# Optimization experiments

Measured on AMD Instinct MI355X. Metric: run time of the kernel, lower is better.

Reference implementation:

```python
import jax, jax.numpy as jnp
import numpy as np
import math

HIDDEN = 1024
HEADS = 16
HEAD_DIM = HIDDEN // HEADS


def setup_inputs() -> dict:
    key = jax.random.key(0)
    ks = jax.random.split(key, 9)
    s = 1.0 / math.sqrt(HIDDEN)
    x = jax.random.normal(ks[0], (4, 2048, HIDDEN), dtype=jnp.float32)
    Wq = jax.random.uniform(ks[1], (HIDDEN, HIDDEN), jnp.float32, -s, s)
    bq = jax.random.uniform(ks[2], (HIDDEN,), jnp.float32, -s, s)
    Wk = jax.random.uniform(ks[3], (HIDDEN, HIDDEN), jnp.float32, -s, s)
    bk = jax.random.uniform(ks[4], (HIDDEN,), jnp.float32, -s, s)
    Wv = jax.random.uniform(ks[5], (HIDDEN, HIDDEN), jnp.float32, -s, s)
    bv = jax.random.uniform(ks[6], (HIDDEN,), jnp.float32, -s, s)
    Wo = jax.random.uniform(ks[7], (HIDDEN, HIDDEN), jnp.float32, -s, s)
    bo = jax.random.uniform(ks[8], (HIDDEN,), jnp.float32, -s, s)
    return {"x": x, "Wq": Wq, "bq": bq, "Wk": Wk, "bk": bk,
            "Wv": Wv, "bv": bv, "Wo": Wo, "bo": bo}


def reference(x, Wq, bq, Wk, bk, Wv, bv, Wo, bo):
    B, T, D = x.shape
    H, Hd = HEADS, HEAD_DIM
    scale = 1.0 / math.sqrt(Hd)
    # projections (torch Linear: y = x @ W.T + b)
    q = (x @ Wq.T + bq).reshape(B, T, H, Hd).transpose(0, 2, 1, 3)  # [B,H,T,Hd]
    k = (x @ Wk.T + bk).reshape(B, T, H, Hd).transpose(0, 2, 1, 3)
    v = (x @ Wv.T + bv).reshape(B, T, H, Hd).transpose(0, 2, 1, 3)
    scores = jnp.einsum("bhqd,bhkd->bhqk", q, k) * scale  # [B,H,T,T]
    attn = jax.nn.softmax(scores, axis=-1)
    out = jnp.einsum("bhqk,bhkd->bhqd", attn, v)  # [B,H,T,Hd]
    out = out.transpose(0, 2, 1, 3).reshape(B, T, D)
    out = out @ Wo.T + bo
    return out.mean(axis=1)  # [B, D]
```

## Files before the change

### kernel.cpp

```cpp
#include <hip/hip_runtime.h>
#include <stdint.h>

#define HIDDEN 1024
#define HEADS 16
#define HEAD_DIM 64
#define BATCH 4
#define SEQ 2048
#define NTOK (BATCH * SEQ)

typedef __attribute__((ext_vector_type(8))) short bf16x8;
typedef __attribute__((ext_vector_type(4))) float floatx4;
typedef __attribute__((ext_vector_type(16))) float floatx16;

#define SCALE_Q 0.18033688011112042f

__device__ __forceinline__ unsigned short f2bf(float f) {
    union { float f; unsigned u; } x; x.f = f;
    unsigned r = x.u + 0x7fffu + ((x.u >> 16) & 1u);
    return (unsigned short)(r >> 16);
}

__device__ __forceinline__ float fast_exp2(float x) {
#if __has_builtin(__builtin_amdgcn_exp2f)
    return __builtin_amdgcn_exp2f(x);
#else
    return exp2f(x);
#endif
}

typedef __attribute__((address_space(3))) unsigned int lds_u32;
typedef const __attribute__((address_space(1))) unsigned int gl_u32;

__device__ __forceinline__ void async_cp16(const void* g, void* l) {
#if __has_builtin(__builtin_amdgcn_global_load_lds)
    __builtin_amdgcn_global_load_lds((gl_u32*)g, (lds_u32*)l, 16, 0, 0);
#else
    *(uint4*)((char*)l + (threadIdx.x & 63) * 16) = *(const uint4*)g;
#endif
}

__global__ __launch_bounds__(256) void conv_all(
    const float* __restrict__ x, const float* __restrict__ Wq,
    const float* __restrict__ Wk, const float* __restrict__ Wv,
    unsigned short* __restrict__ x_bf, unsigned short* __restrict__ wq_bf,
    unsigned short* __restrict__ wk_bf, unsigned short* __restrict__ wv_bf,
    float* __restrict__ accp) {
    const int blk = blockIdx.x, tid = threadIdx.x;
    const float* src;
    unsigned short* dst;
    size_t i;
    if (blk < 8192) {
        src = x; dst = x_bf; i = (size_t)blk * 256 + tid;
        if (blk < 16) accp[blk * 256 + tid] = 0.0f;
    } else {
        int r = blk - 8192;
        int s = r >> 10;
        src = (s == 0) ? Wq : (s == 1) ? Wk : Wv;
        dst = (s == 0) ? wq_bf : (s == 1) ? wk_bf : wv_bf;
        i = (size_t)(r & 1023) * 256 + tid;
    }
    float4 v = *(const float4*)(src + 4 * i);
    unsigned short o[4];
    o[0] = f2bf(v.x); o[1] = f2bf(v.y); o[2] = f2bf(v.z); o[3] = f2bf(v.w);
    *(ushort4*)(dst + 4 * i) = *(ushort4*)o;
}

__global__ __launch_bounds__(256, 3) void qkv_gemm(
    const unsigned short* __restrict__ X,
    const unsigned short* __restrict__ W0, const unsigned short* __restrict__ W1,
    const unsigned short* __restrict__ W2,
    const float* __restrict__ b0, const float* __restrict__ b1,
    const float* __restrict__ b2,
    unsigned short* __restrict__ O0, unsigned short* __restrict__ O1,
    unsigned short* __restrict__ O2) {
    __shared__ __align__(16) char smem[34816];
    unsigned short* tbuf = (unsigned short*)smem;

    const int id = blockIdx.x;
    const int mb = id & 63, nzb = id >> 6;
    const int z = nzb >> 3, nz = nzb & 7;
    const int m0 = mb * 128;
    const unsigned short* W = (z == 0) ? W0 : (z == 1) ? W1 : W2;
    const float* bias       = (z == 0) ? b0 : (z == 1) ? b1 : b2;

    const int tid = threadIdx.x, lane = tid & 63, wave = tid >> 6;
    const int wm = (wave & 1) * 64, wn = (wave >> 1) * 64;

    const int srow = lane >> 2;
    const int sxc = ((lane & 3) ^ (srow & 3)) * 8;
    const unsigned short* ga[2];
    const unsigned short* gb[2];
#pragma unroll
    for (int j = 0; j < 2; ++j) {
        ga[j] = X + (size_t)(m0 + wave * 32 + j * 16 + srow) * HIDDEN + sxc;
        gb[j] = W + (size_t)(nz * 128 + wave * 32 + j * 16 + srow) * HIDDEN + sxc;
    }

    floatx4 acc[4][4];
#pragma unroll
    for (int tm = 0; tm < 4; ++tm)
#pragma unroll
        for (int tn = 0; tn < 4; ++tn)
#pragma unroll
            for (int r = 0; r < 4; ++r) acc[tm][tn][r] = 0.f;

#pragma unroll
    for (int j = 0; j < 2; ++j) {
        async_cp16(ga[j], smem + wave * 2048 + j * 1024);
        async_cp16(gb[j], smem + 16384 + wave * 2048 + j * 1024);
        ga[j] += 32; gb[j] += 32;
    }
    __syncthreads();

    const int fr = (lane & 15) * 64 + (((lane >> 4) ^ (lane & 3)) * 16);
    for (int kt = 0; kt < 32; ++kt) {
        const int cur = kt & 1;
        if (kt < 31) {
#pragma unroll
            for (int j = 0; j < 2; ++j) {
                async_cp16(ga[j], smem + (cur ^ 1) * 8192 + wave * 2048 + j * 1024);
                async_cp16(gb[j], smem + 16384 + (cur ^ 1) * 8192 + wave * 2048 + j * 1024);
                ga[j] += 32; gb[j] += 32;
            }
        }
        const char* Ab = smem + cur * 8192;
        const char* Bb = smem + 16384 + cur * 8192;
        bf16x8 af[4], bfr[4];
#pragma unroll
        for (int t = 0; t < 4; ++t) {
            af[t]  = *(bf16x8*)(Ab + (wm + t * 16) * 64 + fr);
            bfr[t] = *(bf16x8*)(Bb + (wn + t * 16) * 64 + fr);
        }
#pragma unroll
        for (int tm = 0; tm < 4; ++tm)
#pragma unroll
            for (int tn = 0; tn < 4; ++tn)
                acc[tm][tn] = __builtin_amdgcn_mfma_f32_16x16x32_bf16(af[tm], bfr[tn], acc[tm][tn], 0, 0, 0);
        if (kt < 31) __syncthreads();
    }

    const int col = lane & 15, rbase = (lane >> 4) * 4;
    __syncthreads();
    if (z == 2) {
#pragma unroll
        for (int tm = 0; tm < 4; ++tm)
#pragma unroll
            for (int tn = 0; tn < 4; ++tn) {
                const int dr = wn + tn * 16 + col;
                const float bs = bias[nz * 128 + dr];
                const int mi0 = wm + tm * 16 + rbase;
                unsigned short vals[4];
#pragma unroll
                for (int r = 0; r < 4; ++r) vals[r] = f2bf(acc[tm][tn][r] + bs);
                *(ushort4*)&tbuf[dr * 136 + mi0] = *(ushort4*)vals;
            }
        __syncthreads();
        const int dr = tid >> 1, seg = tid & 1;
        const int hh = nz * 2 + (dr >> 6), dd = dr & 63;
        const int bb = m0 >> 11, tb = (m0 & (SEQ - 1)) >> 7;
        unsigned short* dst = O2 + (((size_t)bb * HEADS + hh) * HEAD_DIM + dd) * SEQ
                                 + tb * 128 + seg * 64;
        const unsigned short* srcl = &tbuf[dr * 136 + seg * 64];
#pragma unroll
        for (int i = 0; i < 8; ++i)
            *(uint4*)(dst + i * 8) = *(const uint4*)(srcl + i * 8);
    } else {
        unsigned short* O = (z == 0) ? O0 : O1;
        const float sc = (z == 0) ? SCALE_Q : 1.0f;
#pragma unroll
        for (int tm = 0; tm < 4; ++tm)
#pragma unroll
            for (int tn = 0; tn < 4; ++tn) {
                const int nn = wn + tn * 16 + col;
                const float bs = bias[nz * 128 + nn];
                const int mi0 = wm + tm * 16 + rbase;
#pragma unroll
                for (int r = 0; r < 4; ++r)
                    tbuf[(mi0 + r) * 136 + nn] = f2bf((acc[tm][tn][r] + bs) * sc);
            }
        __syncthreads();
        const int r = tid >> 1, seg = tid & 1;
        unsigned short* dst = O + (size_t)(m0 + r) * HIDDEN + nz * 128 + seg * 64;
        const unsigned short* srcl = &tbuf[r * 136 + seg * 64];
#pragma unroll
        for (int i = 0; i < 8; ++i)
            *(uint4*)(dst + i * 8) = *(const uint4*)(srcl + i * 8);
    }
}

__global__ __launch_bounds__(256, 2) void attn_mfma(
    const unsigned short* __restrict__ Q, const unsigned short* __restrict__ K,
    const unsigned short* __restrict__ Vt, float* __restrict__ accp) {
    __shared__ unsigned short Klds[2][8192];
    __shared__ unsigned short Vlds[2][8192];

    const int tid = threadIdx.x, lane = tid & 63, wave = tid >> 6;
    const int lq = lane & 31, g2 = lane >> 5;

    const int f = blockIdx.x;
    const int bh = (f & 7) * 8 + ((f >> 3) & 7);
    const int qc = f >> 6;
    const int b = bh >> 4, h = bh & 15;

    bf16x8 qfrag[2][4];
#pragma unroll
    for (int g = 0; g < 2; ++g) {
        const size_t qb = ((size_t)(b * SEQ + qc * 256 + wave * 64 + g * 32 + lq)) * HIDDEN
                          + h * HEAD_DIM + g2 * 8;
#pragma unroll
        for (int ds = 0; ds < 4; ++ds) qfrag[g][ds] = *(const bf16x8*)&Q[qb + ds * 16];
    }

    const unsigned short* kg[4];
    const unsigned short* vg[4];
    {
        const int kr = lane >> 3;
        const int kc = ((lane & 7) ^ kr) * 8;
#pragma unroll
        for (int j = 0; j < 4; ++j)
            kg[j] = K + ((size_t)(b * SEQ + wave * 32 + j * 8 + kr)) * HIDDEN + h * HEAD_DIM + kc;
#pragma unroll
        for (int j = 0; j < 4; ++j) {
            const int dl = wave * 16 + j * 4 + (lane >> 4);
            const int cc = ((lane & 15) ^ (dl & 15)) * 8;
            vg[j] = Vt + ((size_t)bh * HEAD_DIM + dl) * SEQ + cc;
        }
    }

    floatx16 oacc[2][2], lacc[2];
#pragma unroll
    for (int g = 0; g < 2; ++g)
#pragma unroll
        for (int r = 0; r < 16; ++r) { oacc[g][0][r] = 0.f; oacc[g][1][r] = 0.f; lacc[g][r] = 0.f; }

    bf16x8 ones;
    {
        union { bf16x8 v; unsigned u[4]; } o;
        o.u[0] = o.u[1] = o.u[2] = o.u[3] = 0x3F803F80u;
        ones = o.v;
    }

#pragma unroll
    for (int j = 0; j < 4; ++j) {
        async_cp16(kg[j], (char*)Klds[0] + (wave * 32 + j * 8) * 128);
        async_cp16(vg[j], (char*)Vlds[0] + (wave * 16 + j * 4) * 256);
        kg[j] += 128 * HIDDEN; vg[j] += 128;
    }
    __syncthreads();

    for (int it = 0; it < 16; ++it) {
        const int cur = it & 1;
        if (it < 15) {
#pragma unroll
            for (int j = 0; j < 4; ++j) {
                async_cp16(kg[j], (char*)Klds[cur ^ 1] + (wave * 32 + j * 8) * 128);
                async_cp16(vg[j], (char*)Vlds[cur ^ 1] + (wave * 16 + j * 4) * 256);
                kg[j] += 128 * HIDDEN; vg[j] += 128;
            }
        }
#pragma unroll
        for (int ks4 = 0; ks4 < 4; ++ks4) {
            const int kk = ks4 * 32;
            const int rr = kk + lq;
            bf16x8 kf[4];
#pragma unroll
            for (int ds = 0; ds < 4; ++ds)
                kf[ds] = *(bf16x8*)((char*)Klds[cur] + rr * 128 + (((g2 + 2 * ds) ^ (lq & 7)) * 16));

            unsigned pk[2][8];
#pragma unroll
            for (int g = 0; g < 2; ++g) {
                floatx16 sacc;
#pragma unroll
                for (int r = 0; r < 16; ++r) sacc[r] = 0.f;
#pragma unroll
                for (int ds = 0; ds < 4; ++ds)
                    sacc = __builtin_amdgcn_mfma_f32_32x32x16_bf16(kf[ds], qfrag[g][ds], sacc, 0, 0, 0);
#pragma unroll
                for (int j = 0; j < 8; ++j) {
                    union { float f; unsigned u; } plo, phi;
                    plo.f = fast_exp2(sacc[2 * j]);
                    phi.f = fast_exp2(sacc[2 * j + 1]);
                    pk[g][j] = __builtin_amdgcn_perm(phi.u, plo.u, 0x07060302u);
                }
            }
#pragma unroll
            for (int ks2 = 0; ks2 < 2; ++ks2) {
                bf16x8 vf[2];
#pragma unroll
                for (int nf = 0; nf < 2; ++nf) {
                    const int d = nf * 32 + lq;
                    const int c0 = (4 * ks4 + 2 * ks2) ^ (d & 15);
                    const int c1 = (4 * ks4 + 2 * ks2 + 1) ^ (d & 15);
                    union { uint2 h[2]; bf16x8 v; } u;
                    u.h[0] = *(uint2*)((char*)Vlds[cur] + d * 256 + c0 * 16 + g2 * 8);
                    u.h[1] = *(uint2*)((char*)Vlds[cur] + d * 256 + c1 * 16 + g2 * 8);
                    vf[nf] = u.v;
                }
#pragma unroll
                for (int g = 0; g < 2; ++g) {
                    union { uint4 u; bf16x8 v; } af;
                    af.u.x = pk[g][4 * ks2];
                    af.u.y = pk[g][4 * ks2 + 1];
                    af.u.z = pk[g][4 * ks2 + 2];
                    af.u.w = pk[g][4 * ks2 + 3];
#pragma unroll
                    for (int nf = 0; nf < 2; ++nf)
                        oacc[g][nf] = __builtin_amdgcn_mfma_f32_32x32x16_bf16(af.v, vf[nf], oacc[g][nf], 0, 0, 0);
                    lacc[g] = __builtin_amdgcn_mfma_f32_32x32x16_bf16(af.v, ones, lacc[g], 0, 0, 0);
                }
            }
        }
        if (it < 15) __syncthreads();
    }

#pragma unroll
    for (int g = 0; g < 2; ++g)
#pragma unroll
        for (int nf = 0; nf < 2; ++nf) {
            float v = 0.f;
#pragma unroll
            for (int r = 0; r < 16; ++r) v += oacc[g][nf][r] / lacc[g][r];
            v += __shfl_xor(v, 32, 64);
            if (lane < 32)
                atomicAdd(&accp[b * HIDDEN + h * HEAD_DIM + nf * 32 + lq], v);
        }
}

__global__ __launch_bounds__(256) void out_proj(const float* __restrict__ acc,
                                                const float* __restrict__ Wo,
                                                const float* __restrict__ bo,
                                                float* __restrict__ out) {
    __shared__ float red[256];
    const int n = blockIdx.x * 64 + (threadIdx.x & 63);
    const int ks = threadIdx.x >> 6;
    const int b = blockIdx.y;
    const float* wr = Wo + (size_t)n * HIDDEN + ks * 256;
    const float* ar = acc + b * HIDDEN + ks * 256;
    float s = 0.f;
#pragma unroll 8
    for (int k = 0; k < 256; k += 4) {
        float4 w = *(const float4*)(wr + k);
        float4 a = *(const float4*)(ar + k);
        s += w.x * a.x + w.y * a.y + w.z * a.z + w.w * a.w;
    }
    red[threadIdx.x] = s;
    __syncthreads();
    if (threadIdx.x < 64) {
        float t = red[threadIdx.x] + red[threadIdx.x + 64]
                + red[threadIdx.x + 128] + red[threadIdx.x + 192];
        out[b * HIDDEN + n] = t * (1.0f / (float)SEQ) + bo[n];
    }
}

extern "C" void kernel_launch(void* const* d_in, const int* in_sizes, int n_in,
                              void* d_out, int out_size, void* d_ws, size_t ws_size,
                              hipStream_t stream) {
    const float* x  = (const float*)d_in[0];
    const float* Wq = (const float*)d_in[1];
    const float* bq = (const float*)d_in[2];
    const float* Wk = (const float*)d_in[3];
    const float* bk = (const float*)d_in[4];
    const float* Wv = (const float*)d_in[5];
    const float* bv = (const float*)d_in[6];
    const float* Wo = (const float*)d_in[7];
    const float* bo = (const float*)d_in[8];
    float* out = (float*)d_out;

    char* ws = (char*)d_ws;
    unsigned short* x_bf  = (unsigned short*)(ws);
    unsigned short* wq_bf = (unsigned short*)(ws + 16777216);
    unsigned short* wk_bf = (unsigned short*)(ws + 18874368);
    unsigned short* wv_bf = (unsigned short*)(ws + 20971520);
    unsigned short* q_bf  = (unsigned short*)(ws + 23068672);
    unsigned short* k_bf  = (unsigned short*)(ws + 39845888);
    unsigned short* vt_bf = (unsigned short*)(ws + 56623104);
    float*          accp  = (float*)(ws + 73400320);

    conv_all<<<dim3(8192 + 3072), dim3(256), 0, stream>>>(
        x, Wq, Wk, Wv, x_bf, wq_bf, wk_bf, wv_bf, accp);

    qkv_gemm<<<dim3(1536), dim3(256), 0, stream>>>(
        x_bf, wq_bf, wk_bf, wv_bf, bq, bk, bv, q_bf, k_bf, vt_bf);

    attn_mfma<<<dim3(512), dim3(256), 0, stream>>>(q_bf, k_bf, vt_bf, accp);

    out_proj<<<dim3(16, BATCH), dim3(256), 0, stream>>>(accp, Wo, bo, out);
}
```

Baseline: 255.4 us.

## Halve attention tile sizes to double blocks and occupancy; permute V-transpose LDS rows

The attention kernel now gives each wave 32 queries instead of 64 and streams 64-key tiles instead of 128. This halves LDS and register use, so launch bounds can target 4 blocks per CU and the grid doubles to 1024 blocks. The V tile layout and swizzle are reworked so each V fragment is one 16-byte LDS read. The QKV GEMM's V-transpose store also permutes row indices to reduce LDS bank conflicts. In exchange, K/V traffic per query doubles, and the loop runs twice as many iterations, each with its own barrier.

```diff
diff --git a/kernel.cpp b/kernel.cpp
--- a/kernel.cpp
+++ b/kernel.cpp
@@ -149,10 +149,11 @@
                 const int dr = wn + tn * 16 + col;
                 const float bs = bias[nz * 128 + dr];
                 const int mi0 = wm + tm * 16 + rbase;
+                const int mip = (mi0 & ~12) | ((mi0 & 4) << 1) | ((mi0 & 8) >> 1);
                 unsigned short vals[4];
 #pragma unroll
                 for (int r = 0; r < 4; ++r) vals[r] = f2bf(acc[tm][tn][r] + bs);
-                *(ushort4*)&tbuf[dr * 136 + mi0] = *(ushort4*)vals;
+                *(ushort4*)&tbuf[dr * 136 + mip] = *(ushort4*)vals;
             }
         __syncthreads();
         const int dr = tid >> 1, seg = tid & 1;
@@ -188,11 +189,11 @@
     }
 }
 
-__global__ __launch_bounds__(256, 2) void attn_mfma(
+__global__ __launch_bounds__(256, 4) void attn_mfma(
     const unsigned short* __restrict__ Q, const unsigned short* __restrict__ K,
     const unsigned short* __restrict__ Vt, float* __restrict__ accp) {
-    __shared__ unsigned short Klds[2][8192];
-    __shared__ unsigned short Vlds[2][8192];
+    __shared__ unsigned short Klds[2][4096];
+    __shared__ unsigned short Vlds[2][4096];
 
     const int tid = threadIdx.x, lane = tid & 63, wave = tid >> 6;
     const int lq = lane & 31, g2 = lane >> 5;
@@ -202,36 +203,33 @@
     const int qc = f >> 6;
     const int b = bh >> 4, h = bh & 15;
 
-    bf16x8 qfrag[2][4];
-#pragma unroll
-    for (int g = 0; g < 2; ++g) {
-        const size_t qb = ((size_t)(b * SEQ + qc * 256 + wave * 64 + g * 32 + lq)) * HIDDEN
+    bf16x8 qfrag[4];
+    {
+        const size_t qb = ((size_t)(b * SEQ + qc * 128 + wave * 32 + lq)) * HIDDEN
                           + h * HEAD_DIM + g2 * 8;
 #pragma unroll
-        for (int ds = 0; ds < 4; ++ds) qfrag[g][ds] = *(const bf16x8*)&Q[qb + ds * 16];
-    }
-
-    const unsigned short* kg[4];
-    const unsigned short* vg[4];
+        for (int ds = 0; ds < 4; ++ds) qfrag[ds] = *(const bf16x8*)&Q[qb + ds * 16];
+    }
+
+    const unsigned short* kg[2];
+    const unsigned short* vg[2];
     {
         const int kr = lane >> 3;
         const int kc = ((lane & 7) ^ kr) * 8;
 #pragma unroll
-        for (int j = 0; j < 4; ++j)
-            kg[j] = K + ((size_t)(b * SEQ + wave * 32 + j * 8 + kr)) * HIDDEN + h * HEAD_DIM + kc;
-#pragma unroll
-        for (int j = 0; j < 4; ++j) {
-            const int dl = wave * 16 + j * 4 + (lane >> 4);
-            const int cc = ((lane & 15) ^ (dl & 15)) * 8;
+        for (int j = 0; j < 2; ++j)
+            kg[j] = K + ((size_t)(b * SEQ + wave * 16 + j * 8 + kr)) * HIDDEN + h * HEAD_DIM + kc;
+#pragma unroll
+        for (int j = 0; j < 2; ++j) {
+            const int dl = wave * 16 + j * 8 + (lane >> 3);
+            const int cc = ((lane & 7) ^ (dl & 7)) * 8;
             vg[j] = Vt + ((size_t)bh * HEAD_DIM + dl) * SEQ + cc;
         }
     }
 
-    floatx16 oacc[2][2], lacc[2];
-#pragma unroll
-    for (int g = 0; g < 2; ++g)
-#pragma unroll
-        for (int r = 0; r < 16; ++r) { oacc[g][0][r] = 0.f; oacc[g][1][r] = 0.f; lacc[g][r] = 0.f; }
+    floatx16 oacc[2], lacc;
+#pragma unroll
+    for (int r = 0; r < 16; ++r) { oacc[0][r] = 0.f; oacc[1][r] = 0.f; lacc[r] = 0.f; }
 
     bf16x8 ones;
     {
@@ -241,90 +239,79 @@
     }
 
 #pragma unroll
-    for (int j = 0; j < 4; ++j) {
-        async_cp16(kg[j], (char*)Klds[0] + (wave * 32 + j * 8) * 128);
-        async_cp16(vg[j], (char*)Vlds[0] + (wave * 16 + j * 4) * 256);
-        kg[j] += 128 * HIDDEN; vg[j] += 128;
+    for (int j = 0; j < 2; ++j) {
+        async_cp16(kg[j], (char*)Klds[0] + (wave * 16 + j * 8) * 128);
+        async_cp16(vg[j], (char*)Vlds[0] + (wave * 16 + j * 8) * 128);
+        kg[j] += 64 * HIDDEN; vg[j] += 64;
     }
     __syncthreads();
 
-    for (int it = 0; it < 16; ++it) {
+    for (int it = 0; it < 32; ++it) {
         const int cur = it & 1;
-        if (it < 15) {
-#pragma unroll
-            for (int j = 0; j < 4; ++j) {
-                async_cp16(kg[j], (char*)Klds[cur ^ 1] + (wave * 32 + j * 8) * 128);
-                async_cp16(vg[j], (char*)Vlds[cur ^ 1] + (wave * 16 + j * 4) * 256);
-                kg[j] += 128 * HIDDEN; vg[j] += 128;
-            }
-        }
-#pragma unroll
-        for (int ks4 = 0; ks4 < 4; ++ks4) {
-            const int kk = ks4 * 32;
-            const int rr = kk + lq;
+        if (it < 31) {
+#pragma unroll
+            for (int j = 0; j < 2; ++j) {
+                async_cp16(kg[j], (char*)Klds[cur ^ 1] + (wave * 16 + j * 8) * 128);
+                async_cp16(vg[j], (char*)Vlds[cur ^ 1] + (wave * 16 + j * 8) * 128);
+                kg[j] += 64 * HIDDEN; vg[j] += 64;
+            }
+        }
+#pragma unroll
+        for (int s32 = 0; s32 < 2; ++s32) {
+            const int rr = s32 * 32 + lq;
             bf16x8 kf[4];
 #pragma unroll
             for (int ds = 0; ds < 4; ++ds)
                 kf[ds] = *(bf16x8*)((char*)Klds[cur] + rr * 128 + (((g2 + 2 * ds) ^ (lq & 7)) * 16));
 
-            unsigned pk[2][8];
-#pragma unroll
-            for (int g = 0; g < 2; ++g) {
-                floatx16 sacc;
-#pragma unroll
-                for (int r = 0; r < 16; ++r) sacc[r] = 0.f;
-#pragma unroll
-                for (int ds = 0; ds < 4; ++ds)
-                    sacc = __builtin_amdgcn_mfma_f32_32x32x16_bf16(kf[ds], qfrag[g][ds], sacc, 0, 0, 0);
-#pragma unroll
-                for (int j = 0; j < 8; ++j) {
-                    union { float f; unsigned u; } plo, phi;
-                    plo.f = fast_exp2(sacc[2 * j]);
-                    phi.f = fast_exp2(sacc[2 * j + 1]);
-                    pk[g][j] = __builtin_amdgcn_perm(phi.u, plo.u, 0x07060302u);
-                }
+            floatx16 sacc;
+#pragma unroll
+            for (int r = 0; r < 16; ++r) sacc[r] = 0.f;
+#pragma unroll
+            for (int ds = 0; ds < 4; ++ds)
+                sacc = __builtin_amdgcn_mfma_f32_32x32x16_bf16(kf[ds], qfrag[ds], sacc, 0, 0, 0);
+
+            unsigned pk[8];
+#pragma unroll
+            for (int j = 0; j < 8; ++j) {
+                union { float f; unsigned u; } plo, phi;
+                plo.f = fast_exp2(sacc[2 * j]);
+                phi.f = fast_exp2(sacc[2 * j + 1]);
+                pk[j] = __builtin_amdgcn_perm(phi.u, plo.u, 0x07060302u);
             }
 #pragma unroll
             for (int ks2 = 0; ks2 < 2; ++ks2) {
+                const int s = s32 * 2 + ks2;
                 bf16x8 vf[2];
 #pragma unroll
                 for (int nf = 0; nf < 2; ++nf) {
                     const int d = nf * 32 + lq;
-                    const int c0 = (4 * ks4 + 2 * ks2) ^ (d & 15);
-                    const int c1 = (4 * ks4 + 2 * ks2 + 1) ^ (d & 15);
-                    union { uint2 h[2]; bf16x8 v; } u;
-                    u.h[0] = *(uint2*)((char*)Vlds[cur] + d * 256 + c0 * 16 + g2 * 8);
-                    u.h[1] = *(uint2*)((char*)Vlds[cur] + d * 256 + c1 * 16 + g2 * 8);
-                    vf[nf] = u.v;
+                    const int c = (2 * s + g2) ^ (d & 7);
+                    vf[nf] = *(bf16x8*)((char*)Vlds[cur] + d * 128 + c * 16);
                 }
-#pragma unroll
-                for (int g = 0; g < 2; ++g) {
-                    union { uint4 u; bf16x8 v; } af;
-                    af.u.x = pk[g][4 * ks2];
-                    af.u.y = pk[g][4 * ks2 + 1];
-                    af.u.z = pk[g][4 * ks2 + 2];
-                    af.u.w = pk[g][4 * ks2 + 3];
-#pragma unroll
-                    for (int nf = 0; nf < 2; ++nf)
-                        oacc[g][nf] = __builtin_amdgcn_mfma_f32_32x32x16_bf16(af.v, vf[nf], oacc[g][nf], 0, 0, 0);
-                    lacc[g] = __builtin_amdgcn_mfma_f32_32x32x16_bf16(af.v, ones, lacc[g], 0, 0, 0);
-                }
-            }
-        }
-        if (it < 15) __syncthreads();
-    }
-
-#pragma unroll
-    for (int g = 0; g < 2; ++g)
-#pragma unroll
-        for (int nf = 0; nf < 2; ++nf) {
-            float v = 0.f;
-#pragma unroll
-            for (int r = 0; r < 16; ++r) v += oacc[g][nf][r] / lacc[g][r];
-            v += __shfl_xor(v, 32, 64);
-            if (lane < 32)
-                atomicAdd(&accp[b * HIDDEN + h * HEAD_DIM + nf * 32 + lq], v);
-        }
+                union { uint4 u; bf16x8 v; } af;
+                af.u.x = pk[4 * ks2];
+                af.u.y = pk[4 * ks2 + 1];
+                af.u.z = pk[4 * ks2 + 2];
+                af.u.w = pk[4 * ks2 + 3];
+#pragma unroll
+                for (int nf = 0; nf < 2; ++nf)
+                    oacc[nf] = __builtin_amdgcn_mfma_f32_32x32x16_bf16(af.v, vf[nf], oacc[nf], 0, 0, 0);
+                lacc = __builtin_amdgcn_mfma_f32_32x32x16_bf16(af.v, ones, lacc, 0, 0, 0);
+            }
+        }
+        if (it < 31) __syncthreads();
+    }
+
+#pragma unroll
+    for (int nf = 0; nf < 2; ++nf) {
+        float v = 0.f;
+#pragma unroll
+        for (int r = 0; r < 16; ++r) v += oacc[nf][r] / lacc[r];
+        v += __shfl_xor(v, 32, 64);
+        if (lane < 32)
+            atomicAdd(&accp[b * HIDDEN + h * HEAD_DIM + nf * 32 + lq], v);
+    }
 }
 
 __global__ __launch_bounds__(256) void out_proj(const float* __restrict__ acc,
@@ -383,7 +370,7 @@
     qkv_gemm<<<dim3(1536), dim3(256), 0, stream>>>(
         x_bf, wq_bf, wk_bf, wv_bf, bq, bk, bv, q_bf, k_bf, vt_bf);
 
-    attn_mfma<<<dim3(512), dim3(256), 0, stream>>>(q_bf, k_bf, vt_bf, accp);
+    attn_mfma<<<dim3(1024), dim3(256), 0, stream>>>(q_bf, k_bf, vt_bf, accp);
 
     out_proj<<<dim3(16, BATCH), dim3(256), 0, stream>>>(accp, Wo, bo, out);
 }
```

Result: no change. 250.8 us (-1.8%).
